# Optimization experiments

Measured on AMD Instinct MI355X. Metric: run time of the kernel, lower is better.

Reference implementation:

```python
import jax, jax.numpy as jnp
import numpy as np

B, T, D_MODEL = 4, 4096, 512
HEADS, BUCKET_SIZE, N_HASHES = 8, 64, 4
DIM_HEAD = D_MODEL // HEADS  # 64
D_FFN = 2048
N_BUCKETS = T // BUCKET_SIZE  # 64
SELF_ATTN_VALUE = -5e4  # reformer TOKEN_SELF_ATTN_VALUE


def setup_inputs() -> dict:
    key = jax.random.key(0)
    ks = jax.random.split(key, 16)
    s = 0.02
    return {
        'x': jax.random.normal(ks[0], (B, T, D_MODEL), jnp.float32),
        'rotations': jax.random.normal(ks[1], (DIM_HEAD, N_HASHES, N_BUCKETS // 2), jnp.float32),
        'w_qk': jax.random.normal(ks[2], (D_MODEL, D_MODEL), jnp.float32) * s,
        'w_v': jax.random.normal(ks[3], (D_MODEL, D_MODEL), jnp.float32) * s,
        'w_out': jax.random.normal(ks[4], (D_MODEL, D_MODEL), jnp.float32) * s,
        'b_out': jnp.zeros((D_MODEL,), jnp.float32),
        'ln1_g': jnp.ones((D_MODEL,), jnp.float32),
        'ln1_b': jnp.zeros((D_MODEL,), jnp.float32),
        'w1': jax.random.normal(ks[5], (D_FFN, D_MODEL), jnp.float32) * s,
        'b1': jnp.zeros((D_FFN,), jnp.float32),
        'w2': jax.random.normal(ks[6], (D_MODEL, D_FFN), jnp.float32) * s,
        'b2': jnp.zeros((D_MODEL,), jnp.float32),
        'ln2_g': jnp.ones((D_MODEL,), jnp.float32),
        'ln2_b': jnp.zeros((D_MODEL,), jnp.float32),
    }


def layer_norm(x, g, b, eps=1e-6):
    m = x.mean(-1, keepdims=True)
    v = ((x - m) ** 2).mean(-1, keepdims=True)
    return (x - m) / jnp.sqrt(v + eps) * g + b


def look_one_back(x):
    # concat each chunk with the previous chunk (wrap-around), along in-chunk axis
    prev = jnp.roll(x, 1, axis=1)
    return jnp.concatenate([x, prev], axis=2)


def lsh_attention(qk, v, rotations):
    # qk, v: (bh, t, d) with shared-QK; rotations: (d, n_hashes, n_buckets//2)
    bh, t, d = qk.shape
    # --- hash: random rotations, argmax over [R, -R] ---
    rot = jnp.einsum('btf,fhi->bhti', qk, rotations)
    rot = jnp.concatenate([rot, -rot], axis=-1)        # (bh, H, t, n_buckets)
    buckets = jnp.argmax(rot, axis=-1)                 # (bh, H, t)
    buckets = buckets + (jnp.arange(N_HASHES) * N_BUCKETS)[None, :, None]
    buckets = buckets.reshape(bh, N_HASHES * t)
    # --- sort by (bucket, position) ---
    ticker = jnp.arange(N_HASHES * t)
    buckets_and_t = t * buckets + (ticker % t)[None, :]
    sticker = jnp.argsort(buckets_and_t, axis=-1)      # stable sort
    undo_sort = jnp.argsort(sticker, axis=-1)
    st = sticker % t                                   # original positions, sorted order
    sqk = jnp.take_along_axis(qk, st[..., None], axis=1)
    sv = jnp.take_along_axis(v, st[..., None], axis=1)
    # --- chunk: n_hashes*n_buckets chunks of bucket_size tokens ---
    n_chunks = N_HASHES * N_BUCKETS
    bq_t = st.reshape(bh, n_chunks, -1)
    bqk = sqk.reshape(bh, n_chunks, -1, d)
    bv = sv.reshape(bh, n_chunks, -1, d)
    bk = bqk / jnp.clip(jnp.linalg.norm(bqk, axis=-1, keepdims=True), 1e-6, None)
    bk = look_one_back(bk)
    bv = look_one_back(bv)
    bkv_t = look_one_back(bq_t)
    # --- local attention within chunk (+ previous chunk) ---
    dots = jnp.einsum('bcid,bcjd->bcij', bqk, bk) * (DIM_HEAD ** -0.5)
    self_mask = bq_t[..., None] == bkv_t[..., None, :]
    dots = jnp.where(self_mask, SELF_ATTN_VALUE, dots)
    logits = jax.nn.logsumexp(dots, axis=-1, keepdims=True)
    probs = jnp.exp(dots - logits)
    bo = jnp.einsum('bcij,bcjd->bcid', probs, bv)
    # --- unsort and combine hash rounds by softmax over round logits ---
    so = bo.reshape(bh, N_HASHES * t, d)
    slogits = logits.reshape(bh, N_HASHES * t)
    o = jnp.take_along_axis(so, undo_sort[..., None], axis=1).reshape(bh, N_HASHES, t, d)
    lg = jnp.take_along_axis(slogits, undo_sort, axis=1).reshape(bh, N_HASHES, t, 1)
    w = jnp.exp(lg - jax.nn.logsumexp(lg, axis=1, keepdims=True))
    return (o * w).sum(axis=1)                         # (bh, t, d)


def reference(x, rotations, w_qk, w_v, w_out, b_out, ln1_g, ln1_b, w1, b1, w2, b2, ln2_g, ln2_b):
    b, t, _ = x.shape
    qk = x @ w_qk.T
    v = x @ w_v.T

    def split_heads(u):
        return u.reshape(b, t, HEADS, DIM_HEAD).transpose(0, 2, 1, 3).reshape(b * HEADS, t, DIM_HEAD)

    attn = lsh_attention(split_heads(qk), split_heads(v), rotations)
    attn = attn.reshape(b, HEADS, t, DIM_HEAD).transpose(0, 2, 1, 3).reshape(b, t, D_MODEL)
    attn = attn @ w_out.T + b_out
    # residual + LN (dropout is identity at inference)
    h = layer_norm(attn + x, ln1_g, ln1_b)
    # position-wise FFN with its own residual + LN
    f = jax.nn.relu(h @ w1.T + b1) @ w2.T + b2
    return layer_norm(f + h, ln2_g, ln2_b)
```

## Files before the change

kernel.cpp:

```cpp
#include <hip/hip_runtime.h>
#include <stdint.h>

typedef unsigned short u16;
typedef __attribute__((ext_vector_type(4))) int   i32x4;
typedef __attribute__((ext_vector_type(4))) float f32x4;

__device__ __forceinline__ u16 f2bf(float x){
  unsigned int u = __float_as_uint(x);
  u += 0x7FFFu + ((u >> 16) & 1u);
  return (u16)(u >> 16);
}
__device__ __forceinline__ float bf2f(u16 h){
  return __uint_as_float(((unsigned int)h) << 16);
}
__device__ __forceinline__ unsigned int cvtpk_bf16(float lo, float hi){
  unsigned int r;
  asm("v_cvt_pk_bf16_f32 %0, %1, %2" : "=v"(r) : "v"(lo), "v"(hi));
  return r;
}
__device__ __forceinline__ f32x4 mfma16(i32x4 a, i32x4 b, f32x4 c){
  asm("v_mfma_f32_16x16x32_bf16 %0, %1, %2, %0" : "+v"(c) : "v"(a), "v"(b));
  return c;
}
__device__ __forceinline__ f32x4 acc_fence(f32x4 c){
  asm volatile("s_nop 7\ns_nop 7" : "+v"(c));
  return c;
}
__device__ __forceinline__ void gl_lds16(const void* g, void* l){
  unsigned long long ga = (unsigned long long)g;
  unsigned int la = (unsigned int)(unsigned long long)l;
  __builtin_amdgcn_global_load_lds((const __attribute__((address_space(1))) void*)ga,
                                   (__attribute__((address_space(3))) void*)la, 16, 0, 0);
}
__device__ __forceinline__ int xcd_swz(int f, int n){
  int chunk = n >> 3;
  return (f & 7) * chunk + (f >> 3);
}
__device__ __forceinline__ unsigned int f2mono(float v){
  unsigned int u = __float_as_uint(v);
  return u ^ ((unsigned int)((int)u >> 31) | 0x80000000u);
}
__device__ __forceinline__ float mono2f(unsigned int mu){
  unsigned int u = (mu & 0x80000000u) ? (mu ^ 0x80000000u) : ~mu;
  return __uint_as_float(u);
}
__device__ __forceinline__ unsigned long long shfl_xor_u64(unsigned long long x, int m){
  int lo = __shfl_xor((int)(unsigned int)(x & 0xFFFFFFFFull), m);
  int hi = __shfl_xor((int)(unsigned int)(x >> 32), m);
  return ((unsigned long long)(unsigned int)hi << 32) | (unsigned int)lo;
}

__global__ __launch_bounds__(256) void k_split(const float* __restrict__ in, u16* __restrict__ hi, u16* __restrict__ lo, int n4){
  int i = blockIdx.x*256 + threadIdx.x;
  if (i >= n4) return;
  float4 v = ((const float4*)in)[i];
  ushort4 h, l;
  h.x=f2bf(v.x); l.x=f2bf(v.x - bf2f(h.x));
  h.y=f2bf(v.y); l.y=f2bf(v.y - bf2f(h.y));
  h.z=f2bf(v.z); l.z=f2bf(v.z - bf2f(h.z));
  h.w=f2bf(v.w); l.w=f2bf(v.w - bf2f(h.w));
  ((ushort4*)hi)[i]=h; ((ushort4*)lo)[i]=l;
}

__global__ __launch_bounds__(256) void k_wprep(
    const float* __restrict__ w_qk, const float* __restrict__ w_v,
    const float* __restrict__ w_out, const float* __restrict__ w1,
    const float* __restrict__ w2, const float* __restrict__ rot,
    u16* __restrict__ wqkh, u16* __restrict__ wqkl,
    u16* __restrict__ wvb, u16* __restrict__ wob,
    u16* __restrict__ w1b, u16* __restrict__ w2b,
    u16* __restrict__ rothi, u16* __restrict__ rotlo)
{
  const int bid = blockIdx.x;
  if (bid >= 2816){
    int i = (bid - 2816)*256 + threadIdx.x;
    int d = i & 63, n = i >> 6;
    float v = rot[d*128 + n];
    u16 h = f2bf(v);
    rothi[i] = h; rotlo[i] = f2bf(v - bf2f(h));
    return;
  }
  const int i = bid*256 + threadIdx.x;
  if (i < 65536){
    float4 v = ((const float4*)w_qk)[i];
    ushort4 h, l;
    h.x=f2bf(v.x); l.x=f2bf(v.x - bf2f(h.x));
    h.y=f2bf(v.y); l.y=f2bf(v.y - bf2f(h.y));
    h.z=f2bf(v.z); l.z=f2bf(v.z - bf2f(h.z));
    h.w=f2bf(v.w); l.w=f2bf(v.w - bf2f(h.w));
    ((ushort4*)wqkh)[i]=h; ((ushort4*)wqkl)[i]=l;
    return;
  }
  const float* src; u16* dst; int j;
  if (i < 131072){ src = w_v;  dst = wvb; j = i - 65536; }
  else if (i < 196608){ src = w_out; dst = wob; j = i - 131072; }
  else if (i < 458752){ src = w1;   dst = w1b; j = i - 196608; }
  else { src = w2; dst = w2b; j = i - 458752; }
  float4 v = ((const float4*)src)[j];
  ushort4 o; o.x=f2bf(v.x); o.y=f2bf(v.y); o.z=f2bf(v.z); o.w=f2bf(v.w);
  ((ushort4*)dst)[j] = o;
}

template<int MODE>
__global__ __launch_bounds__(256) void k_gemm(
    const u16* __restrict__ A0, const u16* __restrict__ B0,
    const float* __restrict__ bias,
    float* __restrict__ Cf, u16* __restrict__ Cb,
    int M, int N, int K)
{
  const int tid = threadIdx.x;
  const int l = tid & 63, w = tid >> 6;
  const int lr = l & 15, lg = l >> 4;
  int flat = blockIdx.y * gridDim.x + blockIdx.x;
  flat = xcd_swz(flat, gridDim.x * gridDim.y);
  const int m0 = (flat / gridDim.x) * 128, n0 = (flat % gridDim.x) * 128;
  const int mbase = (w >> 1) * 64, nbase = (w & 1) * 64;

  __shared__ __align__(16) u16 As[128*64];
  __shared__ __align__(16) u16 Bs[128*64];

  f32x4 zero = {0.f,0.f,0.f,0.f};
  f32x4 acc[4][4];
  #pragma unroll
  for (int i=0;i<4;i++)
    #pragma unroll
    for (int j=0;j<4;j++) acc[i][j] = zero;

  const int row_s = tid >> 3;
  const int c16   = tid & 7;

  for (int k0 = 0; k0 < K; k0 += 64){
    #pragma unroll
    for (int q=0;q<4;q++){
      int ra = q*32 + row_s;
      int cs = c16 ^ (ra & 7);
      gl_lds16(A0 + (size_t)(m0 + ra)*K + k0 + cs*8, (char*)As + q*4096 + tid*16);
      gl_lds16(B0 + (size_t)(n0 + ra)*K + k0 + cs*8, (char*)Bs + q*4096 + tid*16);
    }
    __syncthreads();
    #pragma unroll
    for (int kk=0; kk<64; kk+=32){
      i32x4 af[4], bfr[4];
      #pragma unroll
      for (int mf=0;mf<4;mf++){
        int row = mbase + mf*16 + lr;
        af[mf] = *(const i32x4*)((const char*)As + row*128 + (((kk*2) + (lg*16)) ^ ((row&7)<<4)));
      }
      #pragma unroll
      for (int nf=0;nf<4;nf++){
        int row = nbase + nf*16 + lr;
        bfr[nf] = *(const i32x4*)((const char*)Bs + row*128 + (((kk*2) + (lg*16)) ^ ((row&7)<<4)));
      }
      #pragma unroll
      for (int mf=0;mf<4;mf++)
        #pragma unroll
        for (int nf=0;nf<4;nf++)
          acc[mf][nf] = mfma16(af[mf], bfr[nf], acc[mf][nf]);
    }
    __syncthreads();
  }

  #pragma unroll
  for (int mf=0;mf<4;mf++){
    #pragma unroll
    for (int nf=0;nf<4;nf++){
      f32x4 v = acc_fence(acc[mf][nf]);
      #pragma unroll
      for (int r=0;r<4;r++){
        int m = m0 + mbase + mf*16 + lg*4 + r;
        int n = n0 + nbase + nf*16 + lr;
        float val = v[r];
        if (MODE == 0){
          if (bias) val += bias[n];
          Cf[(size_t)m*N + n] = val;
        } else if (MODE == 1){
          val += bias[n];
          val = fmaxf(val, 0.f);
          Cb[(size_t)m*N + n] = f2bf(val);
        } else {
          int b = m >> 12, t = m & 4095, h = n >> 6, d = n & 63;
          size_t idx = ((((size_t)(b*8 + h)) << 12) + t)*64 + d;
          Cb[idx] = f2bf(val);
        }
      }
    }
  }
}

__global__ __launch_bounds__(256) void k_gemmqk(
    const u16* __restrict__ Ah, const u16* __restrict__ Al,
    const u16* __restrict__ Bh, const u16* __restrict__ Bl,
    u16* __restrict__ qb, u16* __restrict__ qlo, u16* __restrict__ kn)
{
  const int K = 512;
  const int tid = threadIdx.x;
  const int l = tid & 63, w = tid >> 6;
  const int lr = l & 15, lg = l >> 4;
  int flat = blockIdx.y * gridDim.x + blockIdx.x;
  flat = xcd_swz(flat, gridDim.x * gridDim.y);
  const int m0 = (flat >> 2) * 128, n0 = (flat & 3) * 128;
  const int mbase = (w >> 1) * 64, nbase = (w & 1) * 64;

  __shared__ __align__(16) u16 AsH[128*64];
  __shared__ __align__(16) u16 AsL[128*64];
  __shared__ __align__(16) u16 BsH[128*64];
  __shared__ __align__(16) u16 BsL[128*64];

  f32x4 zero = {0.f,0.f,0.f,0.f};
  f32x4 acc[4][4];
  #pragma unroll
  for (int i=0;i<4;i++)
    #pragma unroll
    for (int j=0;j<4;j++) acc[i][j] = zero;

  const int row_s = tid >> 3;
  const int c16   = tid & 7;

  for (int k0 = 0; k0 < K; k0 += 64){
    #pragma unroll
    for (int q=0;q<4;q++){
      int ra = q*32 + row_s;
      int cs = c16 ^ (ra & 7);
      size_t ao = (size_t)(m0 + ra)*K + k0 + cs*8;
      size_t bo = (size_t)(n0 + ra)*K + k0 + cs*8;
      gl_lds16(Ah + ao, (char*)AsH + q*4096 + tid*16);
      gl_lds16(Al + ao, (char*)AsL + q*4096 + tid*16);
      gl_lds16(Bh + bo, (char*)BsH + q*4096 + tid*16);
      gl_lds16(Bl + bo, (char*)BsL + q*4096 + tid*16);
    }
    __syncthreads();
    #pragma unroll
    for (int kk=0; kk<64; kk+=32){
      i32x4 ah[4], al[4], bh2[4], bl2[4];
      #pragma unroll
      for (int mf=0;mf<4;mf++){
        int row = mbase + mf*16 + lr;
        int off = (((kk*2) + (lg*16)) ^ ((row&7)<<4));
        ah[mf] = *(const i32x4*)((const char*)AsH + row*128 + off);
        al[mf] = *(const i32x4*)((const char*)AsL + row*128 + off);
      }
      #pragma unroll
      for (int nf=0;nf<4;nf++){
        int row = nbase + nf*16 + lr;
        int off = (((kk*2) + (lg*16)) ^ ((row&7)<<4));
        bh2[nf] = *(const i32x4*)((const char*)BsH + row*128 + off);
        bl2[nf] = *(const i32x4*)((const char*)BsL + row*128 + off);
      }
      #pragma unroll
      for (int mf=0;mf<4;mf++)
        #pragma unroll
        for (int nf=0;nf<4;nf++){
          acc[mf][nf] = mfma16(ah[mf], bh2[nf], acc[mf][nf]);
          acc[mf][nf] = mfma16(al[mf], bh2[nf], acc[mf][nf]);
          acc[mf][nf] = mfma16(ah[mf], bl2[nf], acc[mf][nf]);
        }
    }
    __syncthreads();
  }

  const int hh = (n0 + nbase) >> 6;
  #pragma unroll
  for (int mf=0;mf<4;mf++){
    f32x4 v[4];
    #pragma unroll
    for (int nf=0;nf<4;nf++) v[nf] = acc_fence(acc[mf][nf]);
    #pragma unroll
    for (int r=0;r<4;r++){
      float ss = 0.f;
      #pragma unroll
      for (int nf=0;nf<4;nf++) ss += v[nf][r]*v[nf][r];
      ss += __shfl_xor(ss, 1); ss += __shfl_xor(ss, 2);
      ss += __shfl_xor(ss, 4); ss += __shfl_xor(ss, 8);
      float scale = 0.18033688f / fmaxf(sqrtf(ss), 1e-6f);
      int m = m0 + mbase + mf*16 + lg*4 + r;
      int b = m >> 12, t = m & 4095;
      size_t rowb = ((((size_t)(b*8 + hh)) << 12) + t) * 64;
      #pragma unroll
      for (int nf=0;nf<4;nf++){
        float val = v[nf][r];
        u16 hbf = f2bf(val);
        size_t idx = rowb + nf*16 + lr;
        qb [idx] = hbf;
        qlo[idx] = f2bf(val - bf2f(hbf));
        kn [idx] = f2bf(val * scale);
      }
    }
  }
}

__global__ __launch_bounds__(256) void k_hash2(
    const u16* __restrict__ qh, const u16* __restrict__ ql,
    const u16* __restrict__ rh, const u16* __restrict__ rl,
    int* __restrict__ bkt)
{
  const int tid = threadIdx.x;
  const int l = tid & 63, w = tid >> 6, lr = l & 15, lg = l >> 4;
  __shared__ __align__(16) u16 Rh[128*64];
  __shared__ __align__(16) u16 Rl[128*64];
  {
    const int row_s = tid >> 3, c8 = tid & 7;
    #pragma unroll
    for (int q = 0; q < 4; q++){
      int ra = q*32 + row_s;
      int cs = c8 ^ (ra & 7);
      gl_lds16(rh + ra*64 + cs*8, (char*)Rh + q*4096 + tid*16);
      gl_lds16(rl + ra*64 + cs*8, (char*)Rl + q*4096 + tid*16);
    }
  }
  const int blk = xcd_swz(blockIdx.x, gridDim.x);
  const int qrow = blk*64 + w*16 + lr;
  const size_t qoff = (size_t)qrow*64;
  i32x4 qhf[2], qlf[2];
  qhf[0] = *(const i32x4*)(qh + qoff + lg*8);
  qhf[1] = *(const i32x4*)(qh + qoff + 32 + lg*8);
  qlf[0] = *(const i32x4*)(ql + qoff + lg*8);
  qlf[1] = *(const i32x4*)(ql + qoff + 32 + lg*8);
  __syncthreads();

  f32x4 zero = {0.f,0.f,0.f,0.f};
  f32x4 acc[8];
  #pragma unroll
  for (int i=0;i<8;i++) acc[i] = zero;
  #pragma unroll
  for (int ks = 0; ks < 2; ks++){
    #pragma unroll
    for (int nf = 0; nf < 8; nf++){
      int row = nf*16 + lr;
      int off = (ks*64 + lg*16) ^ ((row & 7) << 4);
      i32x4 rhf = *(const i32x4*)((const char*)Rh + row*128 + off);
      i32x4 rlf = *(const i32x4*)((const char*)Rl + row*128 + off);
      acc[nf] = mfma16(rhf, qhf[ks], acc[nf]);
      acc[nf] = mfma16(rlf, qhf[ks], acc[nf]);
      acc[nf] = mfma16(rhf, qlf[ks], acc[nf]);
    }
  }

  const int bh = qrow >> 12, t = qrow & 4095;
  #pragma unroll
  for (int hh = 0; hh < 4; hh++){
    f32x4 v0 = acc_fence(acc[2*hh]);
    f32x4 v1 = acc_fence(acc[2*hh+1]);
    unsigned long long kmax = 0, kmin = 0;
    #pragma unroll
    for (int r = 0; r < 4; r++){
      int j0 = lg*4 + r, j1 = 16 + lg*4 + r;
      unsigned int mu0 = f2mono(v0[r]), mu1 = f2mono(v1[r]);
      unsigned long long a = ((unsigned long long)mu0 << 32) | (unsigned int)(31 - j0);
      unsigned long long b = ((unsigned long long)mu1 << 32) | (unsigned int)(31 - j1);
      if (a > kmax) kmax = a;
      if (b > kmax) kmax = b;
      unsigned long long c = ((unsigned long long)(~mu0) << 32) | (unsigned int)(31 - j0);
      unsigned long long d = ((unsigned long long)(~mu1) << 32) | (unsigned int)(31 - j1);
      if (c > kmin) kmin = c;
      if (d > kmin) kmin = d;
    }
    #pragma unroll
    for (int msk = 16; msk < 64; msk <<= 1){
      unsigned long long o1 = shfl_xor_u64(kmax, msk); if (o1 > kmax) kmax = o1;
      unsigned long long o2 = shfl_xor_u64(kmin, msk); if (o2 > kmin) kmin = o2;
    }
    if (lg == 0){
      float vmax = mono2f((unsigned int)(kmax >> 32));
      int jmax = 31 - (int)(kmax & 0xFFFFFFFFull);
      float vmin = mono2f(~(unsigned int)(kmin >> 32));
      int jmin = 31 - (int)(kmin & 0xFFFFFFFFull);
      int bucket = (vmax >= -vmin) ? jmax : 32 + jmin;
      bkt[((size_t)(bh*4 + hh) << 12) + t] = bucket;
    }
  }
}

__global__ __launch_bounds__(64) void k_sort(const int* __restrict__ buckets, int* __restrict__ st){
  const int grp = blockIdx.x;
  const int t = threadIdx.x;
  __shared__ int bkL[4096];
  __shared__ int hist[64][65];
  __shared__ int tot[64];
  const size_t gbase = ((size_t)grp) << 12;
  for (int i=0;i<64;i++)
    bkL[i*64 + t] = buckets[gbase + i*64 + t];
  #pragma unroll
  for (int b=0;b<64;b++) hist[t][b] = 0;
  __syncthreads();
  for (int i=0;i<64;i++){
    int b = bkL[t*64 + i];
    hist[t][b]++;
  }
  __syncthreads();
  { int run = 0;
    for (int tt=0; tt<64; tt++){ int v = hist[tt][t]; hist[tt][t] = run; run += v; }
    tot[t] = run; }
  __syncthreads();
  { int v = tot[t]; int incl = v;
    #pragma unroll
    for (int d=1; d<64; d<<=1){ int n = __shfl_up(incl, d, 64); if (t >= d) incl += n; }
    tot[t] = incl - v; }
  __syncthreads();
  const size_t obase = (((size_t)(grp>>2)) << 14) + ((size_t)(grp&3) << 12);
  for (int i=0;i<64;i++){
    int e = t*64 + i;
    int b = bkL[e];
    int dest = tot[b] + hist[t][b];
    hist[t][b]++;
    st[obase + dest] = e;
  }
}

__global__ __launch_bounds__(256, 4) void k_attn(
    const u16* __restrict__ qb, const u16* __restrict__ kn, const u16* __restrict__ vB,
    const int* __restrict__ st, float* __restrict__ lgt_out, u16* __restrict__ bo)
{
  int flat = blockIdx.y * gridDim.x + blockIdx.x;
  flat = xcd_swz(flat, gridDim.x * gridDim.y);
  const int c = flat & 255, bh = flat >> 8;
  const int rnd = c >> 6;
  const int tid = threadIdx.x;
  const int l = tid & 63, w = tid >> 6, lr = l & 15, lg = l >> 4;

  __shared__ __align__(16) u16 Ks[128*64];
  __shared__ __align__(16) u16 Vt[64][136];
  __shared__ int posk[128];

  if (tid < 128){
    int cc = (tid < 64) ? c : ((c + 255) & 255);
    posk[tid] = st[(((size_t)bh) << 14) + (cc << 6) + (tid & 63)];
  }
  __syncthreads();

  const size_t kvbase = ((size_t)bh) << 12;

  {
    const int rsub = l >> 3, c8 = l & 7;
    #pragma unroll
    for (int q2 = 0; q2 < 4; q2++){
      int row = w*32 + q2*8 + rsub;
      int cs = c8 ^ (row & 7);
      gl_lds16(kn + (kvbase + posk[row])*64 + cs*8,
               (char*)Ks + (w*4 + q2)*1024 + l*16);
    }
  }

  const int pos_q16 = posk[w*16 + lr];
  i32x4 qf[2];
  #pragma unroll
  for (int ks = 0; ks < 2; ks++)
    qf[ks] = *(const i32x4*)(qb + (kvbase + pos_q16)*64 + ks*32 + lg*8);

  {
    const int pp = tid & 63, db = tid >> 6;
    const int q5 = pp & 15;
    const int K0 = (pp >> 4)*32 + 16*((q5 >> 1) & 1) + 4*(q5 >> 2) + 2*(q5 & 1);
    const u16* r0 = vB + (kvbase + posk[K0])*64 + db*16;
    const u16* r1 = vB + (kvbase + posk[K0+1])*64 + db*16;
    uint4 a0 = *(const uint4*)r0, a1 = *(const uint4*)(r0 + 8);
    uint4 b0 = *(const uint4*)r1, b1 = *(const uint4*)(r1 + 8);
    uint av[8] = {a0.x,a0.y,a0.z,a0.w,a1.x,a1.y,a1.z,a1.w};
    uint bv[8] = {b0.x,b0.y,b0.z,b0.w,b1.x,b1.y,b1.z,b1.w};
    #pragma unroll
    for (int dd = 0; dd < 16; dd++){
      uint lo = (av[dd>>1] >> ((dd&1)*16)) & 0xFFFFu;
      uint hi = (bv[dd>>1] >> ((dd&1)*16)) & 0xFFFFu;
      *(uint*)((char*)&Vt[db*16 + dd][0] + pp*4) = lo | (hi << 16);
    }
  }
  __syncthreads();

  f32x4 zero = {0.f,0.f,0.f,0.f};
  f32x4 s[8];
  #pragma unroll
  for (int i=0;i<8;i++) s[i] = zero;
  __builtin_amdgcn_s_setprio(1);
  #pragma unroll
  for (int ks = 0; ks < 2; ks++){
    #pragma unroll
    for (int nf = 0; nf < 8; nf++){
      int row = nf*16 + lr;
      i32x4 kf = *(const i32x4*)((const char*)Ks + row*128 + ((ks*64 + lg*16) ^ ((row&7)<<4)));
      s[nf] = mfma16(kf, qf[ks], s[nf]);
    }
  }
  __builtin_amdgcn_s_setprio(0);

  const bool bdry = (c & 63) == 0;
  float p[8][4];
  float sum = 0.f;
  #pragma unroll
  for (int nf=0;nf<8;nf++){
    f32x4 t = acc_fence(s[nf]);
    #pragma unroll
    for (int r=0;r<4;r++){
      float e = __builtin_amdgcn_exp2f(t[r]);
      if (nf == w && (lg*4 + r) == lr) e = 0.f;
      if (nf >= 4 && bdry && posk[nf*16 + lg*4 + r] == pos_q16) e = 0.f;
      p[nf][r] = e;
      sum += e;
    }
  }
  sum += __shfl_xor(sum, 16);
  sum += __shfl_xor(sum, 32);
  float lv = logf(sum);
  float inv = 1.f / sum;
  if (l < 16)
    lgt_out[(((size_t)(bh*4 + rnd)) << 12) + pos_q16] = lv;

  i32x4 pa[4];
  #pragma unroll
  for (int ks=0;ks<4;ks++){
    uint w0 = cvtpk_bf16(p[2*ks][0],   p[2*ks][1]);
    uint w1 = cvtpk_bf16(p[2*ks][2],   p[2*ks][3]);
    uint w2 = cvtpk_bf16(p[2*ks+1][0], p[2*ks+1][1]);
    uint w3 = cvtpk_bf16(p[2*ks+1][2], p[2*ks+1][3]);
    i32x4 t = {(int)w0,(int)w1,(int)w2,(int)w3};
    pa[ks] = t;
  }

  f32x4 o[4];
  #pragma unroll
  for (int i=0;i<4;i++) o[i] = zero;
  __builtin_amdgcn_s_setprio(1);
  #pragma unroll
  for (int ks=0;ks<4;ks++){
    #pragma unroll
    for (int nf=0;nf<4;nf++){
      i32x4 vf = *(const i32x4*)((const char*)&Vt[nf*16 + lr][0] + ks*64 + lg*16);
      o[nf] = mfma16(pa[ks], vf, o[nf]);
    }
  }
  __builtin_amdgcn_s_setprio(0);
  float invq[4];
  #pragma unroll
  for (int r=0;r<4;r++) invq[r] = __shfl(inv, lg*4 + r, 64);
  #pragma unroll
  for (int nf=0;nf<4;nf++){
    f32x4 ov = acc_fence(o[nf]);
    #pragma unroll
    for (int r=0;r<4;r++){
      int q = w*16 + lg*4 + r;
      bo[((((size_t)(bh*4 + rnd)) << 12) + posk[q])*64 + nf*16 + lr] = f2bf(ov[r] * invq[r]);
    }
  }
}

__global__ __launch_bounds__(256) void k_combine(const u16* __restrict__ bo, const float* __restrict__ lgt,
                                                 u16* __restrict__ attn){
  const int wid = blockIdx.x * 4 + (threadIdx.x >> 6);
  const int l = threadIdx.x & 63;
  const int bh = wid >> 12, t = wid & 4095;
  const size_t lbase = (((size_t)bh) << 14) + t;
  float l0 = lgt[lbase], l1 = lgt[lbase + 4096], l2 = lgt[lbase + 8192], l3 = lgt[lbase + 12288];
  float m = fmaxf(fmaxf(l0,l1), fmaxf(l2,l3));
  float w0 = __expf(l0-m), w1 = __expf(l1-m), w2 = __expf(l2-m), w3 = __expf(l3-m);
  float inv = 1.f / (w0+w1+w2+w3);
  const size_t bbase = ((((size_t)bh) << 14) + t) * 64 + l;
  float o = w0 * bf2f(bo[bbase])
          + w1 * bf2f(bo[bbase + (size_t)4096*64])
          + w2 * bf2f(bo[bbase + (size_t)8192*64])
          + w3 * bf2f(bo[bbase + (size_t)12288*64]);
  o *= inv;
  int b = bh >> 3, h = bh & 7;
  attn[((((size_t)b) << 12) + t) * 512 + h*64 + l] = f2bf(o);
}

template<int WB16>
__global__ __launch_bounds__(256) void k_ln(const float* __restrict__ a,
                                            const float* __restrict__ resf, const u16* __restrict__ resb,
                                            const float* __restrict__ g, const float* __restrict__ bb,
                                            float* __restrict__ of, u16* __restrict__ ob){
  const int row = blockIdx.x*4 + (threadIdx.x >> 6);
  const int l = threadIdx.x & 63;
  const size_t base = (size_t)row*512 + l*8;
  float4 a0 = *(const float4*)(a + base);
  float4 a1 = *(const float4*)(a + base + 4);
  float rv[8];
  if (WB16){
    float4 r0 = *(const float4*)(resf + base);
    float4 r1 = *(const float4*)(resf + base + 4);
    rv[0]=r0.x; rv[1]=r0.y; rv[2]=r0.z; rv[3]=r0.w;
    rv[4]=r1.x; rv[5]=r1.y; rv[6]=r1.z; rv[7]=r1.w;
  } else {
    uint4 rr = *(const uint4*)(resb + base);
    uint rw[4] = {rr.x, rr.y, rr.z, rr.w};
    #pragma unroll
    for (int j=0;j<4;j++){
      rv[2*j]   = bf2f((u16)(rw[j] & 0xFFFF));
      rv[2*j+1] = bf2f((u16)(rw[j] >> 16));
    }
  }
  float v[8] = {a0.x+rv[0], a0.y+rv[1], a0.z+rv[2], a0.w+rv[3],
                a1.x+rv[4], a1.y+rv[5], a1.z+rv[6], a1.w+rv[7]};
  float sum = 0.f;
  #pragma unroll
  for (int j=0;j<8;j++) sum += v[j];
  #pragma unroll
  for (int msk=1; msk<64; msk<<=1) sum += __shfl_xor(sum, msk);
  float mean = sum * (1.f/512.f);
  float ss = 0.f;
  #pragma unroll
  for (int j=0;j<8;j++){ float d = v[j]-mean; ss += d*d; }
  #pragma unroll
  for (int msk=1; msk<64; msk<<=1) ss += __shfl_xor(ss, msk);
  float rstd = rsqrtf(ss * (1.f/512.f) + 1e-6f);
  float4 g0 = *(const float4*)(g + l*8),  g1 = *(const float4*)(g + l*8 + 4);
  float4 b0 = *(const float4*)(bb + l*8), b1 = *(const float4*)(bb + l*8 + 4);
  float gv[8] = {g0.x,g0.y,g0.z,g0.w,g1.x,g1.y,g1.z,g1.w};
  float bv[8] = {b0.x,b0.y,b0.z,b0.w,b1.x,b1.y,b1.z,b1.w};
  float y[8];
  #pragma unroll
  for (int j=0;j<8;j++) y[j] = (v[j]-mean)*rstd*gv[j] + bv[j];
  if (WB16){
    #pragma unroll
    for (int j=0;j<8;j++) ob[base+j] = f2bf(y[j]);
  } else {
    #pragma unroll
    for (int j=0;j<8;j++) of[base+j] = y[j];
  }
}

extern "C" void kernel_launch(void* const* d_in, const int* in_sizes, int n_in,
                              void* d_out, int out_size, void* d_ws, size_t ws_size,
                              hipStream_t stream) {
  const float* x     = (const float*)d_in[0];
  const float* rot   = (const float*)d_in[1];
  const float* w_qk  = (const float*)d_in[2];
  const float* w_v   = (const float*)d_in[3];
  const float* w_out = (const float*)d_in[4];
  const float* b_out = (const float*)d_in[5];
  const float* ln1_g = (const float*)d_in[6];
  const float* ln1_b = (const float*)d_in[7];
  const float* w1    = (const float*)d_in[8];
  const float* b1    = (const float*)d_in[9];
  const float* w2    = (const float*)d_in[10];
  const float* b2    = (const float*)d_in[11];
  const float* ln2_g = (const float*)d_in[12];
  const float* ln2_b = (const float*)d_in[13];
  float* out = (float*)d_out;

  char* p = (char*)d_ws;
  u16*   xh   = (u16*)(p);
  u16*   xl   = (u16*)(p + 16777216);
  u16*   wqkh = (u16*)(p + 33554432);
  u16*   wqkl = (u16*)(p + 34078720);
  u16*   wvb  = (u16*)(p + 34603008);
  u16*   wob  = (u16*)(p + 35127296);
  u16*   w1b  = (u16*)(p + 35651584);
  u16*   w2b  = (u16*)(p + 37748736);
  u16*   qbuf = (u16*)(p + 39845888);
  u16*   knb  = (u16*)(p + 56623104);
  u16*   vb   = (u16*)(p + 73400320);
  int*   bkt  = (int*)(p + 90177536);
  int*   stb  = (int*)(p + 92274688);
  float* lgt  = (float*)(p + 94371840);
  u16*   bo   = (u16*)(p + 96468992);
  u16*   qlo   = bo;
  u16*   rothi = (u16*)(p + 96468992 + 16777216);
  u16*   rotlo = (u16*)(p + 96468992 + 16777216 + 16384);
  u16*   attnc = xl;
  u16*   hb    = xh;
  u16*   hid   = bo;

  k_split<<<8192, 256, 0, stream>>>(x, xh, xl, 16384*512/4);
  k_wprep<<<2848, 256, 0, stream>>>(w_qk, w_v, w_out, w1, w2, rot,
                                    wqkh, wqkl, wvb, wob, w1b, w2b, rothi, rotlo);
  k_gemmqk<<<dim3(4,128), 256, 0, stream>>>(xh, xl, wqkh, wqkl, qbuf, qlo, knb);
  k_gemm<3><<<dim3(4,128), 256, 0, stream>>>(xh, wvb, nullptr, nullptr, vb, 16384, 512, 512);
  k_hash2<<<2048, 256, 0, stream>>>(qbuf, qlo, rothi, rotlo, bkt);
  k_sort<<<128, 64, 0, stream>>>(bkt, stb);
  k_attn<<<dim3(256,32), 256, 0, stream>>>(qbuf, knb, vb, stb, lgt, bo);
  k_combine<<<32768, 256, 0, stream>>>(bo, lgt, attnc);
  k_gemm<0><<<dim3(4,128), 256, 0, stream>>>(attnc, wob, b_out, out, nullptr, 16384, 512, 512);
  k_ln<1><<<4096, 256, 0, stream>>>(out, x, nullptr, ln1_g, ln1_b, nullptr, hb);
  k_gemm<1><<<dim3(16,128), 256, 0, stream>>>(hb, w1b, b1, nullptr, hid, 16384, 2048, 512);
  k_gemm<0><<<dim3(4,128), 256, 0, stream>>>(hid, w2b, b2, out, nullptr, 16384, 512, 2048);
  k_ln<0><<<4096, 256, 0, stream>>>(out, nullptr, hb, ln2_g, ln2_b, out, nullptr);
}
```

Measured before the change: 300.1 us.

## Fuse LSH hashing into QK GEMM, interleave attention outputs, bf16 GEMM outputs

The rotation hash is folded into the QK projection kernel's epilogue, which removes the separate hash kernel and its re-read of q. Attention now reads sorted positions straight from global memory instead of staging them in LDS, swizzles the V-transpose LDS layout, and raises the occupancy hint. Logits and per-round outputs are stored interleaved so the combine step reads contiguous data. The output-projection and FFN2 GEMMs now write bf16 that the layer norms consume, which halves intermediate traffic at some precision cost. The fused epilogue re-reads q from global right after writing it, relying on a vmcnt wait within the same block.

Result: faster. 286.0 us (-4.7%).

```diff
diff --git a/kernel.cpp b/kernel.cpp
--- a/kernel.cpp
+++ b/kernel.cpp
@@ -170,12 +170,12 @@
         int m = m0 + mbase + mf*16 + lg*4 + r;
         int n = n0 + nbase + nf*16 + lr;
         float val = v[r];
-        if (MODE == 0){
-          if (bias) val += bias[n];
-          Cf[(size_t)m*N + n] = val;
-        } else if (MODE == 1){
+        if (MODE == 1){
           val += bias[n];
           val = fmaxf(val, 0.f);
+          Cb[(size_t)m*N + n] = f2bf(val);
+        } else if (MODE == 4){
+          val += bias[n];
           Cb[(size_t)m*N + n] = f2bf(val);
         } else {
           int b = m >> 12, t = m & 4095, h = n >> 6, d = n & 63;
@@ -190,7 +190,9 @@
 __global__ __launch_bounds__(256) void k_gemmqk(
     const u16* __restrict__ Ah, const u16* __restrict__ Al,
     const u16* __restrict__ Bh, const u16* __restrict__ Bl,
-    u16* __restrict__ qb, u16* __restrict__ qlo, u16* __restrict__ kn)
+    const u16* __restrict__ rotH, const u16* __restrict__ rotL,
+    u16* __restrict__ qb, u16* __restrict__ qlo, u16* __restrict__ kn,
+    int* __restrict__ Bkt)
 {
   const int K = 512;
   const int tid = threadIdx.x;
@@ -258,7 +260,9 @@
     __syncthreads();
   }
 
-  const int hh = (n0 + nbase) >> 6;
+  const int head = (n0 + nbase) >> 6;
+  const int b = m0 >> 12;
+  const int t0 = (m0 & 4095) + mbase;
   #pragma unroll
   for (int mf=0;mf<4;mf++){
     f32x4 v[4];
@@ -272,9 +276,8 @@
       ss += __shfl_xor(ss, 1); ss += __shfl_xor(ss, 2);
       ss += __shfl_xor(ss, 4); ss += __shfl_xor(ss, 8);
       float scale = 0.18033688f / fmaxf(sqrtf(ss), 1e-6f);
-      int m = m0 + mbase + mf*16 + lg*4 + r;
-      int b = m >> 12, t = m & 4095;
-      size_t rowb = ((((size_t)(b*8 + hh)) << 12) + t) * 64;
+      int t = t0 + mf*16 + lg*4 + r;
+      size_t rowb = ((((size_t)(b*8 + head)) << 12) + t) * 64;
       #pragma unroll
       for (int nf=0;nf<4;nf++){
         float val = v[nf][r];
@@ -286,86 +289,76 @@
       }
     }
   }
-}
-
-__global__ __launch_bounds__(256) void k_hash2(
-    const u16* __restrict__ qh, const u16* __restrict__ ql,
-    const u16* __restrict__ rh, const u16* __restrict__ rl,
-    int* __restrict__ bkt)
-{
-  const int tid = threadIdx.x;
-  const int l = tid & 63, w = tid >> 6, lr = l & 15, lg = l >> 4;
-  __shared__ __align__(16) u16 Rh[128*64];
-  __shared__ __align__(16) u16 Rl[128*64];
-  {
-    const int row_s = tid >> 3, c8 = tid & 7;
-    #pragma unroll
-    for (int q = 0; q < 4; q++){
-      int ra = q*32 + row_s;
-      int cs = c8 ^ (ra & 7);
-      gl_lds16(rh + ra*64 + cs*8, (char*)Rh + q*4096 + tid*16);
-      gl_lds16(rl + ra*64 + cs*8, (char*)Rl + q*4096 + tid*16);
-    }
-  }
-  const int blk = xcd_swz(blockIdx.x, gridDim.x);
-  const int qrow = blk*64 + w*16 + lr;
-  const size_t qoff = (size_t)qrow*64;
-  i32x4 qhf[2], qlf[2];
-  qhf[0] = *(const i32x4*)(qh + qoff + lg*8);
-  qhf[1] = *(const i32x4*)(qh + qoff + 32 + lg*8);
-  qlf[0] = *(const i32x4*)(ql + qoff + lg*8);
-  qlf[1] = *(const i32x4*)(ql + qoff + 32 + lg*8);
-  __syncthreads();
-
-  f32x4 zero = {0.f,0.f,0.f,0.f};
-  f32x4 acc[8];
-  #pragma unroll
-  for (int i=0;i<8;i++) acc[i] = zero;
-  #pragma unroll
-  for (int ks = 0; ks < 2; ks++){
-    #pragma unroll
-    for (int nf = 0; nf < 8; nf++){
-      int row = nf*16 + lr;
-      int off = (ks*64 + lg*16) ^ ((row & 7) << 4);
-      i32x4 rhf = *(const i32x4*)((const char*)Rh + row*128 + off);
-      i32x4 rlf = *(const i32x4*)((const char*)Rl + row*128 + off);
-      acc[nf] = mfma16(rhf, qhf[ks], acc[nf]);
-      acc[nf] = mfma16(rlf, qhf[ks], acc[nf]);
-      acc[nf] = mfma16(rhf, qlf[ks], acc[nf]);
-    }
-  }
-
-  const int bh = qrow >> 12, t = qrow & 4095;
-  #pragma unroll
-  for (int hh = 0; hh < 4; hh++){
-    f32x4 v0 = acc_fence(acc[2*hh]);
-    f32x4 v1 = acc_fence(acc[2*hh+1]);
-    unsigned long long kmax = 0, kmin = 0;
-    #pragma unroll
-    for (int r = 0; r < 4; r++){
-      int j0 = lg*4 + r, j1 = 16 + lg*4 + r;
-      unsigned int mu0 = f2mono(v0[r]), mu1 = f2mono(v1[r]);
-      unsigned long long a = ((unsigned long long)mu0 << 32) | (unsigned int)(31 - j0);
-      unsigned long long b = ((unsigned long long)mu1 << 32) | (unsigned int)(31 - j1);
-      if (a > kmax) kmax = a;
-      if (b > kmax) kmax = b;
-      unsigned long long c = ((unsigned long long)(~mu0) << 32) | (unsigned int)(31 - j0);
-      unsigned long long d = ((unsigned long long)(~mu1) << 32) | (unsigned int)(31 - j1);
-      if (c > kmin) kmin = c;
-      if (d > kmin) kmin = d;
-    }
-    #pragma unroll
-    for (int msk = 16; msk < 64; msk <<= 1){
-      unsigned long long o1 = shfl_xor_u64(kmax, msk); if (o1 > kmax) kmax = o1;
-      unsigned long long o2 = shfl_xor_u64(kmin, msk); if (o2 > kmin) kmin = o2;
-    }
-    if (lg == 0){
-      float vmax = mono2f((unsigned int)(kmax >> 32));
-      int jmax = 31 - (int)(kmax & 0xFFFFFFFFull);
-      float vmin = mono2f(~(unsigned int)(kmin >> 32));
-      int jmin = 31 - (int)(kmin & 0xFFFFFFFFull);
-      int bucket = (vmax >= -vmin) ? jmax : 32 + jmin;
-      bkt[((size_t)(bh*4 + hh) << 12) + t] = bucket;
+
+  asm volatile("s_waitcnt vmcnt(0)" ::: "memory");
+  const size_t qrow0 = (((size_t)(b*8 + head)) << 12) + t0;
+  i32x4 qhf[2][4], qlf[2][4];
+  #pragma unroll
+  for (int ks=0; ks<2; ks++)
+    #pragma unroll
+    for (int nt=0; nt<4; nt++){
+      size_t off = (qrow0 + nt*16 + lr)*64 + ks*32 + lg*8;
+      qhf[ks][nt] = *(const i32x4*)(qb + off);
+      qlf[ks][nt] = *(const i32x4*)(qlo + off);
+    }
+  #pragma unroll
+  for (int half=0; half<2; half++){
+    f32x4 hacc[4][4];
+    #pragma unroll
+    for (int i=0;i<4;i++)
+      #pragma unroll
+      for (int j=0;j<4;j++) hacc[i][j] = zero;
+    #pragma unroll
+    for (int ks=0; ks<2; ks++){
+      #pragma unroll
+      for (int mf2=0; mf2<4; mf2++){
+        int rowr = half*64 + mf2*16 + lr;
+        i32x4 rh = *(const i32x4*)(rotH + rowr*64 + ks*32 + lg*8);
+        i32x4 rl = *(const i32x4*)(rotL + rowr*64 + ks*32 + lg*8);
+        #pragma unroll
+        for (int nt=0; nt<4; nt++){
+          hacc[mf2][nt] = mfma16(rh, qhf[ks][nt], hacc[mf2][nt]);
+          hacc[mf2][nt] = mfma16(rl, qhf[ks][nt], hacc[mf2][nt]);
+          hacc[mf2][nt] = mfma16(rh, qlf[ks][nt], hacc[mf2][nt]);
+        }
+      }
+    }
+    #pragma unroll
+    for (int g=0; g<2; g++){
+      int hh = half*2 + g;
+      #pragma unroll
+      for (int nt=0; nt<4; nt++){
+        f32x4 v0 = acc_fence(hacc[2*g][nt]);
+        f32x4 v1 = acc_fence(hacc[2*g+1][nt]);
+        unsigned long long kmax = 0, kmin = 0;
+        #pragma unroll
+        for (int r = 0; r < 4; r++){
+          int j0 = lg*4 + r, j1 = 16 + lg*4 + r;
+          unsigned int mu0 = f2mono(v0[r]), mu1 = f2mono(v1[r]);
+          unsigned long long a = ((unsigned long long)mu0 << 32) | (unsigned int)(31 - j0);
+          unsigned long long b2 = ((unsigned long long)mu1 << 32) | (unsigned int)(31 - j1);
+          if (a > kmax) kmax = a;
+          if (b2 > kmax) kmax = b2;
+          unsigned long long c2 = ((unsigned long long)(~mu0) << 32) | (unsigned int)(31 - j0);
+          unsigned long long d2 = ((unsigned long long)(~mu1) << 32) | (unsigned int)(31 - j1);
+          if (c2 > kmin) kmin = c2;
+          if (d2 > kmin) kmin = d2;
+        }
+        #pragma unroll
+        for (int msk = 16; msk < 64; msk <<= 1){
+          unsigned long long o1 = shfl_xor_u64(kmax, msk); if (o1 > kmax) kmax = o1;
+          unsigned long long o2 = shfl_xor_u64(kmin, msk); if (o2 > kmin) kmin = o2;
+        }
+        if (lg == 0){
+          float vmax = mono2f((unsigned int)(kmax >> 32));
+          int jmax = 31 - (int)(kmax & 0xFFFFFFFFull);
+          float vmin = mono2f(~(unsigned int)(kmin >> 32));
+          int jmin = 31 - (int)(kmin & 0xFFFFFFFFull);
+          int bucket = (vmax >= -vmin) ? jmax : 32 + jmin;
+          int t = t0 + nt*16 + lr;
+          Bkt[((size_t)((b*8 + head)*4 + hh) << 12) + t] = bucket;
+        }
+      }
     }
   }
 }
@@ -406,7 +399,7 @@
   }
 }
 
-__global__ __launch_bounds__(256, 4) void k_attn(
+__global__ __launch_bounds__(256, 5) void k_attn(
     const u16* __restrict__ qb, const u16* __restrict__ kn, const u16* __restrict__ vB,
     const int* __restrict__ st, float* __restrict__ lgt_out, u16* __restrict__ bo)
 {
@@ -414,19 +407,14 @@
   flat = xcd_swz(flat, gridDim.x * gridDim.y);
   const int c = flat & 255, bh = flat >> 8;
   const int rnd = c >> 6;
+  const int cprev = (c + 255) & 255;
   const int tid = threadIdx.x;
   const int l = tid & 63, w = tid >> 6, lr = l & 15, lg = l >> 4;
 
   __shared__ __align__(16) u16 Ks[128*64];
-  __shared__ __align__(16) u16 Vt[64][136];
-  __shared__ int posk[128];
-
-  if (tid < 128){
-    int cc = (tid < 64) ? c : ((c + 255) & 255);
-    posk[tid] = st[(((size_t)bh) << 14) + (cc << 6) + (tid & 63)];
-  }
-  __syncthreads();
-
+  __shared__ __align__(16) u16 Vt[64*128];
+
+  const size_t stbase = ((size_t)bh) << 14;
   const size_t kvbase = ((size_t)bh) << 12;
 
   {
@@ -434,13 +422,15 @@
     #pragma unroll
     for (int q2 = 0; q2 < 4; q2++){
       int row = w*32 + q2*8 + rsub;
+      int cc = (row < 64) ? c : cprev;
+      int pos = st[stbase + (cc << 6) + (row & 63)];
       int cs = c8 ^ (row & 7);
-      gl_lds16(kn + (kvbase + posk[row])*64 + cs*8,
+      gl_lds16(kn + (kvbase + pos)*64 + cs*8,
                (char*)Ks + (w*4 + q2)*1024 + l*16);
     }
   }
 
-  const int pos_q16 = posk[w*16 + lr];
+  const int pos_q16 = st[stbase + (c << 6) + (w*16 + lr)];
   i32x4 qf[2];
   #pragma unroll
   for (int ks = 0; ks < 2; ks++)
@@ -450,8 +440,11 @@
     const int pp = tid & 63, db = tid >> 6;
     const int q5 = pp & 15;
     const int K0 = (pp >> 4)*32 + 16*((q5 >> 1) & 1) + 4*(q5 >> 2) + 2*(q5 & 1);
-    const u16* r0 = vB + (kvbase + posk[K0])*64 + db*16;
-    const u16* r1 = vB + (kvbase + posk[K0+1])*64 + db*16;
+    int cc0 = (K0 < 64) ? c : cprev;
+    int p0 = st[stbase + (cc0 << 6) + (K0 & 63)];
+    int p1 = st[stbase + (cc0 << 6) + ((K0 + 1) & 63)];
+    const u16* r0 = vB + (kvbase + p0)*64 + db*16;
+    const u16* r1 = vB + (kvbase + p1)*64 + db*16;
     uint4 a0 = *(const uint4*)r0, a1 = *(const uint4*)(r0 + 8);
     uint4 b0 = *(const uint4*)r1, b1 = *(const uint4*)(r1 + 8);
     uint av[8] = {a0.x,a0.y,a0.z,a0.w,a1.x,a1.y,a1.z,a1.w};
@@ -460,8 +453,18 @@
     for (int dd = 0; dd < 16; dd++){
       uint lo = (av[dd>>1] >> ((dd&1)*16)) & 0xFFFFu;
       uint hi = (bv[dd>>1] >> ((dd&1)*16)) & 0xFFFFu;
-      *(uint*)((char*)&Vt[db*16 + dd][0] + pp*4) = lo | (hi << 16);
-    }
+      int row = db*16 + dd;
+      *(uint*)((char*)Vt + row*256 + ((pp*4) ^ ((row & 7) << 5))) = lo | (hi << 16);
+    }
+  }
+  const bool bdry = (c & 63) == 0;
+  int pkprev[4][4];
+  if (bdry){
+    #pragma unroll
+    for (int nf2=0; nf2<4; nf2++)
+      #pragma unroll
+      for (int r=0;r<4;r++)
+        pkprev[nf2][r] = st[stbase + (cprev << 6) + nf2*16 + lg*4 + r];
   }
   __syncthreads();
 
@@ -481,7 +484,6 @@
   }
   __builtin_amdgcn_s_setprio(0);
 
-  const bool bdry = (c & 63) == 0;
   float p[8][4];
   float sum = 0.f;
   #pragma unroll
@@ -491,7 +493,7 @@
     for (int r=0;r<4;r++){
       float e = __builtin_amdgcn_exp2f(t[r]);
       if (nf == w && (lg*4 + r) == lr) e = 0.f;
-      if (nf >= 4 && bdry && posk[nf*16 + lg*4 + r] == pos_q16) e = 0.f;
+      if (nf >= 4 && bdry && pkprev[nf-4][r] == pos_q16) e = 0.f;
       p[nf][r] = e;
       sum += e;
     }
@@ -501,7 +503,7 @@
   float lv = logf(sum);
   float inv = 1.f / sum;
   if (l < 16)
-    lgt_out[(((size_t)(bh*4 + rnd)) << 12) + pos_q16] = lv;
+    lgt_out[((((size_t)bh) << 12) + pos_q16)*4 + rnd] = lv;
 
   i32x4 pa[4];
   #pragma unroll
@@ -522,21 +524,24 @@
   for (int ks=0;ks<4;ks++){
     #pragma unroll
     for (int nf=0;nf<4;nf++){
-      i32x4 vf = *(const i32x4*)((const char*)&Vt[nf*16 + lr][0] + ks*64 + lg*16);
+      int row = nf*16 + lr;
+      i32x4 vf = *(const i32x4*)((const char*)Vt + row*256 + ((ks*64 + lg*16) ^ ((row & 7) << 5)));
       o[nf] = mfma16(pa[ks], vf, o[nf]);
     }
   }
   __builtin_amdgcn_s_setprio(0);
-  float invq[4];
-  #pragma unroll
-  for (int r=0;r<4;r++) invq[r] = __shfl(inv, lg*4 + r, 64);
+  float invq[4]; int posq[4];
+  #pragma unroll
+  for (int r=0;r<4;r++){
+    invq[r] = __shfl(inv, lg*4 + r, 64);
+    posq[r] = __shfl(pos_q16, lg*4 + r, 64);
+  }
   #pragma unroll
   for (int nf=0;nf<4;nf++){
     f32x4 ov = acc_fence(o[nf]);
     #pragma unroll
     for (int r=0;r<4;r++){
-      int q = w*16 + lg*4 + r;
-      bo[((((size_t)(bh*4 + rnd)) << 12) + posk[q])*64 + nf*16 + lr] = f2bf(ov[r] * invq[r]);
+      bo[((((size_t)bh << 12) + posq[r]))*256 + rnd*64 + nf*16 + lr] = f2bf(ov[r] * invq[r]);
     }
   }
 }
@@ -546,33 +551,36 @@
   const int wid = blockIdx.x * 4 + (threadIdx.x >> 6);
   const int l = threadIdx.x & 63;
   const int bh = wid >> 12, t = wid & 4095;
-  const size_t lbase = (((size_t)bh) << 14) + t;
-  float l0 = lgt[lbase], l1 = lgt[lbase + 4096], l2 = lgt[lbase + 8192], l3 = lgt[lbase + 12288];
-  float m = fmaxf(fmaxf(l0,l1), fmaxf(l2,l3));
-  float w0 = __expf(l0-m), w1 = __expf(l1-m), w2 = __expf(l2-m), w3 = __expf(l3-m);
+  const size_t tb = (((size_t)bh) << 12) + t;
+  float4 lg4 = *(const float4*)(lgt + tb*4);
+  float m = fmaxf(fmaxf(lg4.x,lg4.y), fmaxf(lg4.z,lg4.w));
+  float w0 = __expf(lg4.x-m), w1 = __expf(lg4.y-m), w2 = __expf(lg4.z-m), w3 = __expf(lg4.w-m);
   float inv = 1.f / (w0+w1+w2+w3);
-  const size_t bbase = ((((size_t)bh) << 14) + t) * 64 + l;
-  float o = w0 * bf2f(bo[bbase])
-          + w1 * bf2f(bo[bbase + (size_t)4096*64])
-          + w2 * bf2f(bo[bbase + (size_t)8192*64])
-          + w3 * bf2f(bo[bbase + (size_t)12288*64]);
+  const u16* bp = bo + tb*256;
+  float o = w0 * bf2f(bp[l]) + w1 * bf2f(bp[64+l]) + w2 * bf2f(bp[128+l]) + w3 * bf2f(bp[192+l]);
   o *= inv;
   int b = bh >> 3, h = bh & 7;
   attn[((((size_t)b) << 12) + t) * 512 + h*64 + l] = f2bf(o);
 }
 
-template<int WB16>
-__global__ __launch_bounds__(256) void k_ln(const float* __restrict__ a,
+template<int RESF>
+__global__ __launch_bounds__(256) void k_ln(const u16* __restrict__ a,
                                             const float* __restrict__ resf, const u16* __restrict__ resb,
                                             const float* __restrict__ g, const float* __restrict__ bb,
                                             float* __restrict__ of, u16* __restrict__ ob){
   const int row = blockIdx.x*4 + (threadIdx.x >> 6);
   const int l = threadIdx.x & 63;
   const size_t base = (size_t)row*512 + l*8;
-  float4 a0 = *(const float4*)(a + base);
-  float4 a1 = *(const float4*)(a + base + 4);
+  uint4 aa = *(const uint4*)(a + base);
+  uint aw[4] = {aa.x, aa.y, aa.z, aa.w};
+  float av[8];
+  #pragma unroll
+  for (int j=0;j<4;j++){
+    av[2*j]   = bf2f((u16)(aw[j] & 0xFFFF));
+    av[2*j+1] = bf2f((u16)(aw[j] >> 16));
+  }
   float rv[8];
-  if (WB16){
+  if (RESF){
     float4 r0 = *(const float4*)(resf + base);
     float4 r1 = *(const float4*)(resf + base + 4);
     rv[0]=r0.x; rv[1]=r0.y; rv[2]=r0.z; rv[3]=r0.w;
@@ -586,8 +594,9 @@
       rv[2*j+1] = bf2f((u16)(rw[j] >> 16));
     }
   }
-  float v[8] = {a0.x+rv[0], a0.y+rv[1], a0.z+rv[2], a0.w+rv[3],
-                a1.x+rv[4], a1.y+rv[5], a1.z+rv[6], a1.w+rv[7]};
+  float v[8];
+  #pragma unroll
+  for (int j=0;j<8;j++) v[j] = av[j] + rv[j];
   float sum = 0.f;
   #pragma unroll
   for (int j=0;j<8;j++) sum += v[j];
@@ -607,7 +616,7 @@
   float y[8];
   #pragma unroll
   for (int j=0;j<8;j++) y[j] = (v[j]-mean)*rstd*gv[j] + bv[j];
-  if (WB16){
+  if (RESF){
     #pragma unroll
     for (int j=0;j<8;j++) ob[base+j] = f2bf(y[j]);
   } else {
@@ -655,21 +664,23 @@
   u16*   rothi = (u16*)(p + 96468992 + 16777216);
   u16*   rotlo = (u16*)(p + 96468992 + 16777216 + 16384);
   u16*   attnc = xl;
+  u16*   projb = qbuf;
+  u16*   fb    = xl;
   u16*   hb    = xh;
   u16*   hid   = bo;
 
   k_split<<<8192, 256, 0, stream>>>(x, xh, xl, 16384*512/4);
   k_wprep<<<2848, 256, 0, stream>>>(w_qk, w_v, w_out, w1, w2, rot,
                                     wqkh, wqkl, wvb, wob, w1b, w2b, rothi, rotlo);
-  k_gemmqk<<<dim3(4,128), 256, 0, stream>>>(xh, xl, wqkh, wqkl, qbuf, qlo, knb);
+  k_gemmqk<<<dim3(4,128), 256, 0, stream>>>(xh, xl, wqkh, wqkl, rothi, rotlo,
+                                            qbuf, qlo, knb, bkt);
   k_gemm<3><<<dim3(4,128), 256, 0, stream>>>(xh, wvb, nullptr, nullptr, vb, 16384, 512, 512);
-  k_hash2<<<2048, 256, 0, stream>>>(qbuf, qlo, rothi, rotlo, bkt);
   k_sort<<<128, 64, 0, stream>>>(bkt, stb);
   k_attn<<<dim3(256,32), 256, 0, stream>>>(qbuf, knb, vb, stb, lgt, bo);
   k_combine<<<32768, 256, 0, stream>>>(bo, lgt, attnc);
-  k_gemm<0><<<dim3(4,128), 256, 0, stream>>>(attnc, wob, b_out, out, nullptr, 16384, 512, 512);
-  k_ln<1><<<4096, 256, 0, stream>>>(out, x, nullptr, ln1_g, ln1_b, nullptr, hb);
+  k_gemm<4><<<dim3(4,128), 256, 0, stream>>>(attnc, wob, b_out, nullptr, projb, 16384, 512, 512);
+  k_ln<1><<<4096, 256, 0, stream>>>(projb, x, nullptr, ln1_g, ln1_b, nullptr, hb);
   k_gemm<1><<<dim3(16,128), 256, 0, stream>>>(hb, w1b, b1, nullptr, hid, 16384, 2048, 512);
-  k_gemm<0><<<dim3(4,128), 256, 0, stream>>>(hid, w2b, b2, out, nullptr, 16384, 512, 2048);
-  k_ln<0><<<4096, 256, 0, stream>>>(out, nullptr, hb, ln2_g, ln2_b, out, nullptr);
-}
+  k_gemm<4><<<dim3(4,128), 256, 0, stream>>>(hid, w2b, b2, nullptr, fb, 16384, 512, 2048);
+  k_ln<0><<<4096, 256, 0, stream>>>(fb, nullptr, hb, ln2_g, ln2_b, out, nullptr);
+}
```
